# Kernel optimization log

Measured on AMD Instinct MI355X. Metric: run time of the kernel, lower is better.

The kernel has to match this reference:

```python
import jax, jax.numpy as jnp
import numpy as np

BN_EPS = 1e-5


def setup_inputs() -> dict:
    key = jax.random.key(0)
    ks = jax.random.split(key, 8)
    B, C, H, W = 8, 256, 64, 64
    Ci = 128
    x = jax.random.normal(ks[0], (B, C, H, W), dtype=jnp.float32)
    # 1x1 conv weights stored as [out, in] (kernel size 1 squeezed)
    sc = 1.0 / np.sqrt(C)
    g_w = jax.random.uniform(ks[1], (Ci, C), jnp.float32, -sc, sc)
    g_b = jax.random.uniform(ks[2], (Ci,), jnp.float32, -sc, sc)
    theta_w = jax.random.uniform(ks[3], (Ci, C), jnp.float32, -sc, sc)
    theta_b = jax.random.uniform(ks[4], (Ci,), jnp.float32, -sc, sc)
    phi_w = jax.random.uniform(ks[5], (Ci, C), jnp.float32, -sc, sc)
    phi_b = jax.random.uniform(ks[6], (Ci,), jnp.float32, -sc, sc)
    # W conv: normal(std=0.01) weight, zero bias (per _init_weights)
    W_w = 0.01 * jax.random.normal(ks[7], (C, Ci), dtype=jnp.float32)
    W_b = jnp.zeros((C,), dtype=jnp.float32)
    bn_gamma = jnp.ones((C,), dtype=jnp.float32)
    bn_beta = jnp.zeros((C,), dtype=jnp.float32)
    return {"x": x, "g_w": g_w, "g_b": g_b, "theta_w": theta_w, "theta_b": theta_b,
            "phi_w": phi_w, "phi_b": phi_b, "W_w": W_w, "W_b": W_b,
            "bn_gamma": bn_gamma, "bn_beta": bn_beta}


def reference(x, g_w, g_b, theta_w, theta_b, phi_w, phi_b, W_w, W_b, bn_gamma, bn_beta):
    B, C, H, W = x.shape
    xf = x.reshape(B, C, H * W)                                   # [B, C, N]
    # 1x1 convs == per-position channel GEMMs
    g_x = jnp.einsum('oc,bcn->bon', g_w, xf) + g_b[:, None]        # [B, Ci, N]
    th = jnp.einsum('oc,bcn->bon', theta_w, xf) + theta_b[:, None]
    ph = jnp.einsum('oc,bcn->bon', phi_w, xf) + phi_b[:, None]
    # theta^T phi : [B, N, N] dense attention scores
    f = jnp.einsum('bcn,bcm->bnm', th, ph)
    attn = jax.nn.softmax(f, axis=-1)
    # attention-weighted sum of g values -> [B, Ci, N]
    y = jnp.einsum('bnm,bcm->bcn', attn, g_x)
    # output 1x1 conv + BatchNorm2d (training-mode batch stats)
    wy = jnp.einsum('oc,bcn->bon', W_w, y) + W_b[:, None]          # [B, C, N]
    mean = jnp.mean(wy, axis=(0, 2), keepdims=True)
    var = jnp.var(wy, axis=(0, 2), keepdims=True)
    wy_bn = (wy - mean) * jax.lax.rsqrt(var + BN_EPS)
    wy_bn = wy_bn * bn_gamma[:, None] + bn_beta[:, None]
    z = wy_bn.reshape(B, C, H, W) + x
    return z
```

## Files before the change

### kernel.cpp

```cpp
#include <hip/hip_runtime.h>
#include <hip/hip_bf16.h>
#include <math.h>

#define B_   8
#define C_   256
#define CI_  128
#define N_   4096

typedef unsigned short ushort_t;
typedef unsigned int uint_t;
typedef __attribute__((ext_vector_type(8))) short short8;
typedef __attribute__((ext_vector_type(16))) float floatx16;

#define OFF_W3B  0ull
#define OFF_B3   196608ull
#define OFF_WCB  198144ull
#define OFF_XT   263680ull
#define OFF_THT  17040896ull
#define OFF_PHT  25429504ull
#define OFF_G16  33818112ull
#define OFF_LP   42206720ull
#define OFF_YPB  42468864ull
#define OFF_WY   263680ull
#define OFF_ST   59246080ull

__device__ __forceinline__ ushort_t f2bf(float x) {
  union { float f; uint_t u; } c; c.f = x;
  return (ushort_t)((c.u + 0x7fffu + ((c.u >> 16) & 1u)) >> 16);
}
__device__ __forceinline__ uint_t pkbf(float a, float b) {
  __hip_bfloat162 h = __float22bfloat162_rn(float2{a, b});
  union { __hip_bfloat162 h; uint_t u; } c; c.h = h; return c.u;
}
__device__ __forceinline__ float bf_lo(uint_t u) {
  union { uint_t u; float f; } c; c.u = u << 16; return c.f;
}
__device__ __forceinline__ float bf_hi(uint_t u) {
  union { uint_t u; float f; } c; c.u = u & 0xffff0000u; return c.f;
}
__device__ __forceinline__ void async_copy16(const void* g, void* l) {
  __builtin_amdgcn_global_load_lds(
      (const __attribute__((address_space(1))) unsigned int*)g,
      (__attribute__((address_space(3))) unsigned int*)l, 16, 0, 0);
}

__global__ __launch_bounds__(256) void pack_w(
    const float* __restrict__ g_w, const float* __restrict__ g_b,
    const float* __restrict__ th_w, const float* __restrict__ th_b,
    const float* __restrict__ ph_w, const float* __restrict__ ph_b,
    const float* __restrict__ W_w,
    ushort_t* __restrict__ W3b, float* __restrict__ b3,
    ushort_t* __restrict__ Wc)
{
  int bid = blockIdx.x;
  if (bid < 384) {
    int i = bid * 256 + threadIdx.x;
    int o = i >> 8;
    float v;
    if (o < 128)      v = g_w[i];
    else if (o < 256) v = th_w[i - 128*256];
    else              v = ph_w[i - 256*256];
    W3b[i] = f2bf(v);
    if ((i & 255) == 0)
      b3[o] = (o < 128) ? g_b[o] : (o < 256) ? th_b[o - 128] : ph_b[o - 256];
  } else {
    int j = (bid - 384) * 256 + threadIdx.x;
    Wc[j] = f2bf(W_w[j]);
  }
}

__global__ __launch_bounds__(256) void xcast(
    const float* __restrict__ x, ushort_t* __restrict__ xt)
{
  const int b = blockIdx.z, c0 = blockIdx.y * 64, n0 = blockIdx.x * 64;
  const int tid = threadIdx.x;
  __shared__ float xs[64][65];
  const int nq = (tid & 15) * 4, cr = tid >> 4;
  #pragma unroll
  for (int i = 0; i < 4; ++i) {
    float4 v = *(const float4*)&x[((size_t)b * C_ + c0 + cr + 16*i) * N_ + n0 + nq];
    xs[cr + 16*i][nq] = v.x; xs[cr + 16*i][nq+1] = v.y;
    xs[cr + 16*i][nq+2] = v.z; xs[cr + 16*i][nq+3] = v.w;
  }
  __syncthreads();
  const int n = tid >> 2, cs = (tid & 3) * 16;
  uint_t u[8];
  #pragma unroll
  for (int j = 0; j < 8; ++j)
    u[j] = pkbf(xs[cs + 2*j][n], xs[cs + 2*j + 1][n]);
  ushort_t* dst = &xt[((size_t)b * N_ + n0 + n) * C_ + c0 + cs];
  *(uint4*)dst       = make_uint4(u[0], u[1], u[2], u[3]);
  *(uint4*)(dst + 8) = make_uint4(u[4], u[5], u[6], u[7]);
}

__global__ __launch_bounds__(256, 2) void proj_all(
    const ushort_t* __restrict__ W3b, const float* __restrict__ b3,
    const ushort_t* __restrict__ xt, ushort_t* __restrict__ tht,
    ushort_t* __restrict__ pht, ushort_t* __restrict__ g16)
{
  const int b = blockIdx.z, nb = blockIdx.x, ot = blockIdx.y;
  const int gm = (ot == 2);
  const int o0 = gm ? 0 : (128 + ot * 128);
  const int tid = threadIdx.x, w = tid >> 6, lane = tid & 63;
  const int l31 = lane & 31, h = lane >> 5, xk = l31 & 7;
  __shared__ ushort_t ws_l[128 * 64];
  __shared__ ushort_t xs_l[128 * 64];
  const ushort_t* xb = xt + (size_t)b * N_ * C_;
  const int n0 = nb * 128;
  floatx16 acc[4];
  #pragma unroll
  for (int ct = 0; ct < 4; ++ct)
    #pragma unroll
    for (int r = 0; r < 16; ++r) acc[ct][r] = 0.f;

  const int gr = lane >> 3, gu = lane & 7;
  for (int k0 = 0; k0 < C_; k0 += 64) {
    __syncthreads();
    #pragma unroll
    for (int i = 0; i < 4; ++i) {
      int r = w*32 + i*8 + gr;
      async_copy16(&W3b[(size_t)(o0 + r) * C_ + k0 + ((gu ^ (r & 7)) * 8)],
                   &ws_l[(w*32 + i*8) * 64]);
      async_copy16(&xb[(size_t)(n0 + r) * C_ + k0 + ((gu ^ (r & 7)) * 8)],
                   &xs_l[(w*32 + i*8) * 64]);
    }
    __syncthreads();
    const ushort_t* bmat = gm ? ws_l : xs_l;
    const ushort_t* amat = gm ? xs_l : ws_l;
    #pragma unroll
    for (int kk = 0; kk < 4; ++kk) {
      int fc = ((2*kk + h) ^ xk) * 8;
      short8 bf = *(const short8*)&bmat[(w*32 + l31) * 64 + fc];
      #pragma unroll
      for (int ct = 0; ct < 4; ++ct) {
        short8 af = *(const short8*)&amat[(ct*32 + l31) * 64 + fc];
        acc[ct] = __builtin_amdgcn_mfma_f32_32x32x16_bf16(af, bf, acc[ct], 0, 0, 0);
      }
    }
  }

  if (gm) {
    float bv = b3[w*32 + l31];
    ushort_t* gp = g16 + ((size_t)b * CI_ + w*32 + l31) * N_;
    #pragma unroll
    for (int ct = 0; ct < 4; ++ct)
      #pragma unroll
      for (int rq = 0; rq < 4; ++rq) {
        uint2 d = make_uint2(pkbf(acc[ct][4*rq+0] + bv, acc[ct][4*rq+1] + bv),
                             pkbf(acc[ct][4*rq+2] + bv, acc[ct][4*rq+3] + bv));
        *(uint2*)&gp[n0 + ct*32 + 8*rq + 4*h] = d;
      }
  } else {
    ushort_t* tp = ((ot == 0) ? tht : pht) + ((size_t)b * N_ + n0 + w*32 + l31) * CI_;
    #pragma unroll
    for (int ct = 0; ct < 4; ++ct)
      #pragma unroll
      for (int rq = 0; rq < 4; ++rq) {
        float4 bv = *(const float4*)&b3[o0 + ct*32 + 8*rq + 4*h];
        uint2 d = make_uint2(pkbf(acc[ct][4*rq+0] + bv.x, acc[ct][4*rq+1] + bv.y),
                             pkbf(acc[ct][4*rq+2] + bv.z, acc[ct][4*rq+3] + bv.w));
        *(uint2*)&tp[ct*32 + 8*rq + 4*h] = d;
      }
  }
}

#define LOG2E_  1.442695041f
#define MBIAS_  (-28.85390082f)

__global__ __launch_bounds__(256, 2) void attn_mfma(
    const ushort_t* __restrict__ tht, const ushort_t* __restrict__ pht,
    const ushort_t* __restrict__ g16, ushort_t* __restrict__ yp,
    float* __restrict__ lp)
{
  const int b  = blockIdx.x & 7;
  const int ms = (blockIdx.x >> 3) & 1;
  const int qb = blockIdx.x >> 4;
  const int tid = threadIdx.x, w = tid >> 6, lane = tid & 63;
  const int l31 = lane & 31, h = lane >> 5, xk = l31 & 7;

  __shared__ ushort_t smem[40960];
  ushort_t* Plw = smem + 32768 + w * 2048;

  const int q0w = qb * 128 + w * 32;
  const int m_base = ms * 2048;

  const ushort_t* thb = tht + (size_t)b * N_ * CI_;
  const ushort_t* phb = pht + (size_t)b * N_ * CI_;
  const ushort_t* gbp = g16 + (size_t)b * CI_ * N_;

  short8 tf[8];
  #pragma unroll
  for (int kk = 0; kk < 8; ++kk)
    tf[kk] = *(const short8*)&thb[(size_t)(q0w + l31) * CI_ + kk*16 + h*8];

  floatx16 acc[4];
  #pragma unroll
  for (int ct = 0; ct < 4; ++ct)
    #pragma unroll
    for (int r = 0; r < 16; ++r) acc[ct][r] = 0.f;
  float lpart = 0.f;

  const int phr = lane >> 4, phu = lane & 15;
  const int gr  = lane >> 3, gu  = lane & 7;

  #define STAGE_ATTN(m0v, bufv)                                               \
    {                                                                         \
      ushort_t* phs_ = smem + (bufv) * 8192;                                  \
      ushort_t* gs_  = smem + 16384 + (bufv) * 8192;                          \
      _Pragma("unroll")                                                       \
      for (int i = 0; i < 4; ++i) {                                           \
        int row = w*16 + i*4 + phr;                                           \
        async_copy16(&phb[(size_t)((m0v) + row) * CI_ + ((phu ^ (row & 7)) * 8)], \
                     &phs_[(w*16 + i*4) * 128]);                              \
      }                                                                       \
      _Pragma("unroll")                                                       \
      for (int i = 0; i < 4; ++i) {                                           \
        int c = w*32 + i*8 + gr;                                              \
        async_copy16(&gbp[(size_t)c * N_ + (m0v) + ((gu ^ (c & 7)) * 8)],     \
                     &gs_[(w*32 + i*8) * 64]);                                \
      }                                                                       \
    }

  STAGE_ATTN(m_base, 0);
  asm volatile("s_waitcnt vmcnt(0)" ::: "memory");
  __builtin_amdgcn_s_barrier();

  #pragma unroll 2
  for (int it = 0; it < 32; ++it) {
    const int cur = it & 1;
    const int m0 = m_base + it * 64;
    if (it < 31) STAGE_ATTN(m0 + 64, cur ^ 1);
    const ushort_t* phs = smem + cur * 8192;
    const ushort_t* gs  = smem + 16384 + cur * 8192;

    #pragma unroll
    for (int mt = 0; mt < 2; ++mt) {
      floatx16 s;
      #pragma unroll
      for (int r = 0; r < 16; ++r) s[r] = 0.f;
      __builtin_amdgcn_s_setprio(1);
      #pragma unroll
      for (int kk = 0; kk < 8; ++kk) {
        short8 pf = *(const short8*)&phs[(mt*32 + l31) * 128 + (((2*kk + h) ^ xk) * 8)];
        s = __builtin_amdgcn_mfma_f32_32x32x16_bf16(pf, tf[kk], s, 0, 0, 0);
      }
      __builtin_amdgcn_s_setprio(0);
      float ls = 0.f;
      #pragma unroll
      for (int rq = 0; rq < 4; ++rq) {
        float p0 = exp2f(fmaf(s[4*rq+0], LOG2E_, MBIAS_));
        float p1 = exp2f(fmaf(s[4*rq+1], LOG2E_, MBIAS_));
        float p2 = exp2f(fmaf(s[4*rq+2], LOG2E_, MBIAS_));
        float p3 = exp2f(fmaf(s[4*rq+3], LOG2E_, MBIAS_));
        ls += (p0 + p1) + (p2 + p3);
        uint2 d = make_uint2(pkbf(p0, p1), pkbf(p2, p3));
        *(uint2*)&Plw[l31 * 64 + (((mt*4 + rq) ^ xk) * 8) + h*4] = d;
      }
      lpart += ls;
    }

    __builtin_amdgcn_s_setprio(1);
    #pragma unroll
    for (int kk = 0; kk < 4; ++kk) {
      int pc = ((2*kk + h) ^ xk) * 8;
      short8 pfr = *(const short8*)&Plw[l31 * 64 + pc];
      #pragma unroll
      for (int ct = 0; ct < 4; ++ct) {
        short8 gf = *(const short8*)&gs[(ct*32 + l31) * 64 + pc];
        acc[ct] = __builtin_amdgcn_mfma_f32_32x32x16_bf16(gf, pfr, acc[ct], 0, 0, 0);
      }
    }
    __builtin_amdgcn_s_setprio(0);

    asm volatile("s_waitcnt vmcnt(0)" ::: "memory");
    __builtin_amdgcn_s_barrier();
  }

  float lq = lpart + __shfl_xor(lpart, 32);
  if (h == 0)
    lp[((size_t)ms * 8 + b) * N_ + q0w + l31] = lq;

  __syncthreads();
  ushort_t* tr = smem + w * 4096;
  #pragma unroll
  for (int ct = 0; ct < 4; ++ct)
    #pragma unroll
    for (int rq = 0; rq < 4; ++rq) {
      uint2 d = make_uint2(pkbf(acc[ct][4*rq+0], acc[ct][4*rq+1]),
                           pkbf(acc[ct][4*rq+2], acc[ct][4*rq+3]));
      *(uint2*)&tr[l31 * 128 + ct*32 + 8*rq + 4*h] = d;
    }
  ushort_t* ypb = yp + (((size_t)ms * 8 + b) * N_ + q0w) * CI_;
  #pragma unroll
  for (int itx = 0; itx < 8; ++itx) {
    int row = itx*4 + (lane >> 4);
    int cu  = (lane & 15) * 8;
    uint4 v = *(const uint4*)&tr[row * 128 + cu];
    *(uint4*)&ypb[(size_t)row * CI_ + cu] = v;
  }
}

__global__ __launch_bounds__(256, 2) void wgemm_fused(
    const ushort_t* __restrict__ Wc, const float* __restrict__ Wb,
    const ushort_t* __restrict__ yp, const float* __restrict__ lp,
    float* __restrict__ WY)
{
  const int b = blockIdx.z, nb = blockIdx.x, ot = blockIdx.y;
  const int o0 = ot * 128;
  const int tid = threadIdx.x, w = tid >> 6, lane = tid & 63;
  const int l31 = lane & 31, h = lane >> 5, xk = l31 & 7;
  __shared__ ushort_t ws_l[128 * 64];
  __shared__ ushort_t xs_l[128 * 64];
  const int n0 = nb * 128;
  const size_t PH = (size_t)B_ * N_ * CI_;
  const ushort_t* yp0 = yp + (size_t)b * N_ * CI_;
  const ushort_t* yp1 = yp0 + PH;
  floatx16 acc[4];
  #pragma unroll
  for (int ct = 0; ct < 4; ++ct)
    #pragma unroll
    for (int r = 0; r < 16; ++r) acc[ct][r] = 0.f;

  const int gr = lane >> 3, gu = lane & 7;
  for (int k0 = 0; k0 < CI_; k0 += 64) {
    __syncthreads();
    #pragma unroll
    for (int i = 0; i < 4; ++i) {
      int r = w*32 + i*8 + gr;
      async_copy16(&Wc[(size_t)(o0 + r) * CI_ + k0 + ((gu ^ (r & 7)) * 8)],
                   &ws_l[(w*32 + i*8) * 64]);
      int n = n0 + r;
      size_t src = (size_t)n * CI_ + k0 + ((gu ^ (r & 7)) * 8);
      uint4 a0 = *(const uint4*)&yp0[src];
      uint4 a1 = *(const uint4*)&yp1[src];
      float inv = 1.0f / (lp[(size_t)b * N_ + n] + lp[(size_t)(8 + b) * N_ + n]);
      uint4 o;
      o.x = pkbf((bf_lo(a0.x) + bf_lo(a1.x)) * inv, (bf_hi(a0.x) + bf_hi(a1.x)) * inv);
      o.y = pkbf((bf_lo(a0.y) + bf_lo(a1.y)) * inv, (bf_hi(a0.y) + bf_hi(a1.y)) * inv);
      o.z = pkbf((bf_lo(a0.z) + bf_lo(a1.z)) * inv, (bf_hi(a0.z) + bf_hi(a1.z)) * inv);
      o.w = pkbf((bf_lo(a0.w) + bf_lo(a1.w)) * inv, (bf_hi(a0.w) + bf_hi(a1.w)) * inv);
      *(uint4*)&xs_l[r * 64 + gu * 8] = o;
    }
    __syncthreads();
    #pragma unroll
    for (int kk = 0; kk < 4; ++kk) {
      int fc = ((2*kk + h) ^ xk) * 8;
      short8 bf = *(const short8*)&xs_l[(w*32 + l31) * 64 + fc];
      #pragma unroll
      for (int ct = 0; ct < 4; ++ct) {
        short8 af = *(const short8*)&ws_l[(ct*32 + l31) * 64 + fc];
        acc[ct] = __builtin_amdgcn_mfma_f32_32x32x16_bf16(af, bf, acc[ct], 0, 0, 0);
      }
    }
  }
  const int n = n0 + w*32 + l31;
  #pragma unroll
  for (int ct = 0; ct < 4; ++ct)
    #pragma unroll
    for (int rq = 0; rq < 4; ++rq) {
      float4 bv = *(const float4*)&Wb[o0 + ct*32 + 8*rq + 4*h];
      #pragma unroll
      for (int j = 0; j < 4; ++j) {
        int o = o0 + ct*32 + 8*rq + 4*h + j;
        WY[((size_t)b * C_ + o) * N_ + n] = acc[ct][4*rq + j] + (&bv.x)[j];
      }
    }
}

__global__ __launch_bounds__(256) void bn_stats(
    const float* __restrict__ WY, float* __restrict__ st)
{
  const int o = blockIdx.x;
  const int tid = threadIdx.x;
  float s = 0.f, s2 = 0.f;
  for (int b = 0; b < B_; ++b) {
    const float* p = WY + ((size_t)b * C_ + o) * N_;
    for (int n = tid * 4; n < N_; n += 256 * 4) {
      float4 v = *(const float4*)&p[n];
      s  += v.x + v.y + v.z + v.w;
      s2 += v.x * v.x + v.y * v.y + v.z * v.z + v.w * v.w;
    }
  }
  __shared__ float rs[256], rs2[256];
  rs[tid] = s; rs2[tid] = s2;
  __syncthreads();
  for (int off = 128; off > 0; off >>= 1) {
    if (tid < off) { rs[tid] += rs[tid + off]; rs2[tid] += rs2[tid + off]; }
    __syncthreads();
  }
  if (tid == 0) {
    const float M = (float)(B_ * N_);
    float mean = rs[0] / M;
    float var  = rs2[0] / M - mean * mean;
    st[o] = mean;
    st[256 + o] = rsqrtf(var + 1e-5f);
  }
}

__global__ __launch_bounds__(256) void bn_apply(
    const float* __restrict__ WY, const float* __restrict__ x,
    const float* __restrict__ st, const float* __restrict__ gamma,
    const float* __restrict__ beta, float* __restrict__ out)
{
  size_t i = ((size_t)blockIdx.x * 256 + threadIdx.x) * 4;
  int o = (int)((i >> 12) & 255);
  float4 w  = *(const float4*)&WY[i];
  float4 xv = *(const float4*)&x[i];
  float gsc = gamma[o] * st[256 + o];
  float bb  = beta[o] - st[o] * gsc;
  float4 v;
  v.x = w.x * gsc + bb + xv.x;
  v.y = w.y * gsc + bb + xv.y;
  v.z = w.z * gsc + bb + xv.z;
  v.w = w.w * gsc + bb + xv.w;
  *(float4*)&out[i] = v;
}

extern "C" void kernel_launch(void* const* d_in, const int* in_sizes, int n_in,
                              void* d_out, int out_size, void* d_ws, size_t ws_size,
                              hipStream_t stream)
{
  const float* x       = (const float*)d_in[0];
  const float* g_w     = (const float*)d_in[1];
  const float* g_b     = (const float*)d_in[2];
  const float* theta_w = (const float*)d_in[3];
  const float* theta_b = (const float*)d_in[4];
  const float* phi_w   = (const float*)d_in[5];
  const float* phi_b   = (const float*)d_in[6];
  const float* W_w     = (const float*)d_in[7];
  const float* W_b     = (const float*)d_in[8];
  const float* gamma   = (const float*)d_in[9];
  const float* beta    = (const float*)d_in[10];
  float* out = (float*)d_out;

  char* ws = (char*)d_ws;
  ushort_t* W3b = (ushort_t*)(ws + OFF_W3B);
  float*    b3  = (float*)(ws + OFF_B3);
  ushort_t* Wc  = (ushort_t*)(ws + OFF_WCB);
  ushort_t* xt  = (ushort_t*)(ws + OFF_XT);
  ushort_t* tht = (ushort_t*)(ws + OFF_THT);
  ushort_t* pht = (ushort_t*)(ws + OFF_PHT);
  ushort_t* g16 = (ushort_t*)(ws + OFF_G16);
  float*    lpp = (float*)(ws + OFF_LP);
  ushort_t* ypb = (ushort_t*)(ws + OFF_YPB);
  float*    WY  = (float*)(ws + OFF_WY);
  float*    ST  = (float*)(ws + OFF_ST);

  pack_w<<<512, 256, 0, stream>>>(g_w, g_b, theta_w, theta_b, phi_w, phi_b,
                                  W_w, W3b, b3, Wc);
  xcast<<<dim3(64, 4, 8), 256, 0, stream>>>(x, xt);
  proj_all<<<dim3(32, 3, 8), 256, 0, stream>>>(W3b, b3, xt, tht, pht, g16);
  attn_mfma<<<512, 256, 0, stream>>>(tht, pht, g16, ypb, lpp);
  wgemm_fused<<<dim3(32, 2, 8), 256, 0, stream>>>(Wc, W_b, ypb, lpp, WY);
  bn_stats<<<256, 256, 0, stream>>>(WY, ST);
  bn_apply<<<8192, 256, 0, stream>>>(WY, x, ST, gamma, beta, out);
}
```

Baseline: 243.4 us.

## Keep softmax probabilities in registers via permlane32 swap instead of LDS round-trip

The exponentiated scores are packed to bf16 and rearranged across lane halves with permlane32_swap, so they feed the PV MFMA operand directly without being written to and re-read from shared memory. This removes the per-wave P staging buffer (8K ushorts of LDS) and its stores and loads. The two QK score tiles are also computed interleaved, giving two independent MFMA chains. The costs are extra cross-lane permute instructions and higher register pressure from holding two score accumulators at once.

```diff
diff --git a/kernel.cpp b/kernel.cpp
--- a/kernel.cpp
+++ b/kernel.cpp
@@ -11,6 +11,7 @@
 typedef unsigned int uint_t;
 typedef __attribute__((ext_vector_type(8))) short short8;
 typedef __attribute__((ext_vector_type(16))) float floatx16;
+typedef __attribute__((ext_vector_type(2))) unsigned int uint2v;
 
 #define OFF_W3B  0ull
 #define OFF_B3   196608ull
@@ -178,8 +179,7 @@
   const int tid = threadIdx.x, w = tid >> 6, lane = tid & 63;
   const int l31 = lane & 31, h = lane >> 5, xk = l31 & 7;
 
-  __shared__ ushort_t smem[40960];
-  ushort_t* Plw = smem + 32768 + w * 2048;
+  __shared__ ushort_t smem[32768];
 
   const int q0w = qb * 128 + w * 32;
   const int m_base = ms * 2048;
@@ -221,6 +221,38 @@
       }                                                                       \
     }
 
+  #define SMPV(sv, mtv)                                                       \
+    {                                                                         \
+      uint_t Aw[4], Bw[4];                                                    \
+      float ls = 0.f;                                                         \
+      _Pragma("unroll")                                                       \
+      for (int rq = 0; rq < 4; ++rq) {                                        \
+        float p0 = exp2f(fmaf(sv[4*rq+0], LOG2E_, MBIAS_));                   \
+        float p1 = exp2f(fmaf(sv[4*rq+1], LOG2E_, MBIAS_));                   \
+        float p2 = exp2f(fmaf(sv[4*rq+2], LOG2E_, MBIAS_));                   \
+        float p3 = exp2f(fmaf(sv[4*rq+3], LOG2E_, MBIAS_));                   \
+        ls += (p0 + p1) + (p2 + p3);                                          \
+        Aw[rq] = pkbf(p0, p1);                                                \
+        Bw[rq] = pkbf(p2, p3);                                                \
+      }                                                                       \
+      lpart += ls;                                                            \
+      _Pragma("unroll")                                                       \
+      for (int t = 0; t < 2; ++t) {                                           \
+        uint2v ra = __builtin_amdgcn_permlane32_swap(Aw[2*t], Aw[2*t+1], false, false); \
+        uint2v rb = __builtin_amdgcn_permlane32_swap(Bw[2*t], Bw[2*t+1], false, false); \
+        union { uint_t u[4]; short8 s; } pk_;                                 \
+        pk_.u[0] = ra.x; pk_.u[1] = rb.x; pk_.u[2] = ra.y; pk_.u[3] = rb.y;   \
+        const int pc = ((2*(2*(mtv) + t) + h) ^ xk) * 8;                      \
+        __builtin_amdgcn_s_setprio(1);                                        \
+        _Pragma("unroll")                                                     \
+        for (int ct = 0; ct < 4; ++ct) {                                      \
+          short8 gf = *(const short8*)&gs[(ct*32 + l31) * 64 + pc];           \
+          acc[ct] = __builtin_amdgcn_mfma_f32_32x32x16_bf16(gf, pk_.s, acc[ct], 0, 0, 0); \
+        }                                                                     \
+        __builtin_amdgcn_s_setprio(0);                                        \
+      }                                                                       \
+    }
+
   STAGE_ATTN(m_base, 0);
   asm volatile("s_waitcnt vmcnt(0)" ::: "memory");
   __builtin_amdgcn_s_barrier();
@@ -233,44 +265,22 @@
     const ushort_t* phs = smem + cur * 8192;
     const ushort_t* gs  = smem + 16384 + cur * 8192;
 
-    #pragma unroll
-    for (int mt = 0; mt < 2; ++mt) {
-      floatx16 s;
-      #pragma unroll
-      for (int r = 0; r < 16; ++r) s[r] = 0.f;
-      __builtin_amdgcn_s_setprio(1);
-      #pragma unroll
-      for (int kk = 0; kk < 8; ++kk) {
-        short8 pf = *(const short8*)&phs[(mt*32 + l31) * 128 + (((2*kk + h) ^ xk) * 8)];
-        s = __builtin_amdgcn_mfma_f32_32x32x16_bf16(pf, tf[kk], s, 0, 0, 0);
-      }
-      __builtin_amdgcn_s_setprio(0);
-      float ls = 0.f;
-      #pragma unroll
-      for (int rq = 0; rq < 4; ++rq) {
-        float p0 = exp2f(fmaf(s[4*rq+0], LOG2E_, MBIAS_));
-        float p1 = exp2f(fmaf(s[4*rq+1], LOG2E_, MBIAS_));
-        float p2 = exp2f(fmaf(s[4*rq+2], LOG2E_, MBIAS_));
-        float p3 = exp2f(fmaf(s[4*rq+3], LOG2E_, MBIAS_));
-        ls += (p0 + p1) + (p2 + p3);
-        uint2 d = make_uint2(pkbf(p0, p1), pkbf(p2, p3));
-        *(uint2*)&Plw[l31 * 64 + (((mt*4 + rq) ^ xk) * 8) + h*4] = d;
-      }
-      lpart += ls;
-    }
-
+    floatx16 s0, s1;
+    #pragma unroll
+    for (int r = 0; r < 16; ++r) { s0[r] = 0.f; s1[r] = 0.f; }
     __builtin_amdgcn_s_setprio(1);
     #pragma unroll
-    for (int kk = 0; kk < 4; ++kk) {
-      int pc = ((2*kk + h) ^ xk) * 8;
-      short8 pfr = *(const short8*)&Plw[l31 * 64 + pc];
-      #pragma unroll
-      for (int ct = 0; ct < 4; ++ct) {
-        short8 gf = *(const short8*)&gs[(ct*32 + l31) * 64 + pc];
-        acc[ct] = __builtin_amdgcn_mfma_f32_32x32x16_bf16(gf, pfr, acc[ct], 0, 0, 0);
-      }
+    for (int kk = 0; kk < 8; ++kk) {
+      const int fc = (((2*kk + h) ^ xk) * 8);
+      short8 pf0 = *(const short8*)&phs[(l31) * 128 + fc];
+      s0 = __builtin_amdgcn_mfma_f32_32x32x16_bf16(pf0, tf[kk], s0, 0, 0, 0);
+      short8 pf1 = *(const short8*)&phs[(32 + l31) * 128 + fc];
+      s1 = __builtin_amdgcn_mfma_f32_32x32x16_bf16(pf1, tf[kk], s1, 0, 0, 0);
     }
     __builtin_amdgcn_s_setprio(0);
+
+    SMPV(s0, 0)
+    SMPV(s1, 1)
 
     asm volatile("s_waitcnt vmcnt(0)" ::: "memory");
     __builtin_amdgcn_s_barrier();
```

New measurement: 253.0 us. 4.0% more time.

## Split attention keys four ways, keep P in registers via permlane swap, bf16 WY

Applied to the files above, without the earlier changes.

The attention kernel now splits the key range into four chunks instead of two and uses 32-key tiles, which roughly halves shared memory and raises occupancy to 4 blocks per SU. The softmax probabilities are rearranged with permlane32_swap and fed straight into the PV MFMA, so the LDS round-trip for P goes away. A raw v_exp_f32 replaces exp2f. Row sums are combined with atomicAdd into a buffer that pack_w now zeroes. The output of the W projection is stored as bf16, which halves the traffic for the BN stats and apply passes. In exchange, the four partial y buffers add more reads in wgemm, and storing WY in bf16 lowers precision.

```diff
diff --git a/kernel.cpp b/kernel.cpp
--- a/kernel.cpp
+++ b/kernel.cpp
@@ -11,18 +11,20 @@
 typedef unsigned int uint_t;
 typedef __attribute__((ext_vector_type(8))) short short8;
 typedef __attribute__((ext_vector_type(16))) float floatx16;
-
-#define OFF_W3B  0ull
-#define OFF_B3   196608ull
-#define OFF_WCB  198144ull
-#define OFF_XT   263680ull
-#define OFF_THT  17040896ull
-#define OFF_PHT  25429504ull
-#define OFF_G16  33818112ull
-#define OFF_LP   42206720ull
-#define OFF_YPB  42468864ull
-#define OFF_WY   263680ull
-#define OFF_ST   59246080ull
+typedef __attribute__((ext_vector_type(2))) unsigned int uint2v;
+
+#define OFF_W3B   0ull
+#define OFF_B3    196608ull
+#define OFF_WCB   198144ull
+#define OFF_LP    263680ull
+#define OFF_ST    394752ull
+#define OFF_THT   396800ull
+#define OFF_PHT   8785408ull
+#define OFF_G16   17174016ull
+#define OFF_XT    25562624ull
+#define OFF_YP23  25562624ull
+#define OFF_YP01  42339840ull
+#define OFF_WY    396800ull
 
 __device__ __forceinline__ ushort_t f2bf(float x) {
   union { float f; uint_t u; } c; c.f = x;
@@ -37,6 +39,9 @@
 }
 __device__ __forceinline__ float bf_hi(uint_t u) {
   union { uint_t u; float f; } c; c.u = u & 0xffff0000u; return c.f;
+}
+__device__ __forceinline__ float fexp2(float x) {
+  float r; asm("v_exp_f32 %0, %1\ns_nop 0" : "=v"(r) : "v"(x)); return r;
 }
 __device__ __forceinline__ void async_copy16(const void* g, void* l) {
   __builtin_amdgcn_global_load_lds(
@@ -50,7 +55,7 @@
     const float* __restrict__ ph_w, const float* __restrict__ ph_b,
     const float* __restrict__ W_w,
     ushort_t* __restrict__ W3b, float* __restrict__ b3,
-    ushort_t* __restrict__ Wc)
+    ushort_t* __restrict__ Wc, float* __restrict__ lp)
 {
   int bid = blockIdx.x;
   if (bid < 384) {
@@ -63,9 +68,11 @@
     W3b[i] = f2bf(v);
     if ((i & 255) == 0)
       b3[o] = (o < 128) ? g_b[o] : (o < 256) ? th_b[o - 128] : ph_b[o - 256];
-  } else {
+  } else if (bid < 512) {
     int j = (bid - 384) * 256 + threadIdx.x;
     Wc[j] = f2bf(W_w[j]);
+  } else {
+    lp[(bid - 512) * 256 + threadIdx.x] = 0.f;
   }
 }
 
@@ -167,22 +174,22 @@
 #define LOG2E_  1.442695041f
 #define MBIAS_  (-28.85390082f)
 
-__global__ __launch_bounds__(256, 2) void attn_mfma(
+__global__ __launch_bounds__(256, 4) void attn_mfma(
     const ushort_t* __restrict__ tht, const ushort_t* __restrict__ pht,
-    const ushort_t* __restrict__ g16, ushort_t* __restrict__ yp,
-    float* __restrict__ lp)
+    const ushort_t* __restrict__ g16, ushort_t* __restrict__ ypA,
+    ushort_t* __restrict__ ypB, float* __restrict__ lp)
 {
   const int b  = blockIdx.x & 7;
-  const int ms = (blockIdx.x >> 3) & 1;
-  const int qb = blockIdx.x >> 4;
+  const int ms = (blockIdx.x >> 3) & 3;
+  const int qb = blockIdx.x >> 5;
   const int tid = threadIdx.x, w = tid >> 6, lane = tid & 63;
   const int l31 = lane & 31, h = lane >> 5, xk = l31 & 7;
-
-  __shared__ ushort_t smem[40960];
-  ushort_t* Plw = smem + 32768 + w * 2048;
+  const int xk2 = (l31 >> 1) & 3;
+
+  __shared__ ushort_t smem[16384];
 
   const int q0w = qb * 128 + w * 32;
-  const int m_base = ms * 2048;
+  const int m_base = ms * 1024;
 
   const ushort_t* thb = tht + (size_t)b * N_ * CI_;
   const ushort_t* phb = pht + (size_t)b * N_ * CI_;
@@ -201,23 +208,23 @@
   float lpart = 0.f;
 
   const int phr = lane >> 4, phu = lane & 15;
-  const int gr  = lane >> 3, gu  = lane & 7;
+  const int g_r = lane >> 2, g_u = lane & 3;
 
   #define STAGE_ATTN(m0v, bufv)                                               \
     {                                                                         \
-      ushort_t* phs_ = smem + (bufv) * 8192;                                  \
-      ushort_t* gs_  = smem + 16384 + (bufv) * 8192;                          \
+      ushort_t* phs_ = smem + (bufv) * 4096;                                  \
+      ushort_t* gs_  = smem + 8192 + (bufv) * 4096;                           \
       _Pragma("unroll")                                                       \
-      for (int i = 0; i < 4; ++i) {                                           \
-        int row = w*16 + i*4 + phr;                                           \
+      for (int i = 0; i < 2; ++i) {                                           \
+        int row = w*8 + i*4 + phr;                                            \
         async_copy16(&phb[(size_t)((m0v) + row) * CI_ + ((phu ^ (row & 7)) * 8)], \
-                     &phs_[(w*16 + i*4) * 128]);                              \
+                     &phs_[(w*8 + i*4) * 128]);                               \
       }                                                                       \
       _Pragma("unroll")                                                       \
-      for (int i = 0; i < 4; ++i) {                                           \
-        int c = w*32 + i*8 + gr;                                              \
-        async_copy16(&gbp[(size_t)c * N_ + (m0v) + ((gu ^ (c & 7)) * 8)],     \
-                     &gs_[(w*32 + i*8) * 64]);                                \
+      for (int i = 0; i < 2; ++i) {                                           \
+        int c = (w*2 + i) * 16 + g_r;                                         \
+        async_copy16(&gbp[(size_t)c * N_ + (m0v) + ((g_u ^ ((c >> 1) & 3)) * 8)], \
+                     &gs_[(w*2 + i) * 512]);                                  \
       }                                                                       \
     }
 
@@ -228,49 +235,51 @@
   #pragma unroll 2
   for (int it = 0; it < 32; ++it) {
     const int cur = it & 1;
-    const int m0 = m_base + it * 64;
-    if (it < 31) STAGE_ATTN(m0 + 64, cur ^ 1);
-    const ushort_t* phs = smem + cur * 8192;
-    const ushort_t* gs  = smem + 16384 + cur * 8192;
-
-    #pragma unroll
-    for (int mt = 0; mt < 2; ++mt) {
-      floatx16 s;
-      #pragma unroll
-      for (int r = 0; r < 16; ++r) s[r] = 0.f;
+    const int m0 = m_base + it * 32;
+    if (it < 31) STAGE_ATTN(m0 + 32, cur ^ 1);
+    const ushort_t* phs = smem + cur * 4096;
+    const ushort_t* gs  = smem + 8192 + cur * 4096;
+
+    floatx16 s;
+    #pragma unroll
+    for (int r = 0; r < 16; ++r) s[r] = 0.f;
+    __builtin_amdgcn_s_setprio(1);
+    #pragma unroll
+    for (int kk = 0; kk < 8; ++kk) {
+      short8 pf = *(const short8*)&phs[l31 * 128 + (((2*kk + h) ^ xk) * 8)];
+      s = __builtin_amdgcn_mfma_f32_32x32x16_bf16(pf, tf[kk], s, 0, 0, 0);
+    }
+    __builtin_amdgcn_s_setprio(0);
+
+    uint_t Aw[4], Bw[4];
+    float ls = 0.f;
+    #pragma unroll
+    for (int rq = 0; rq < 4; ++rq) {
+      float p0 = fexp2(fmaf(s[4*rq+0], LOG2E_, MBIAS_));
+      float p1 = fexp2(fmaf(s[4*rq+1], LOG2E_, MBIAS_));
+      float p2 = fexp2(fmaf(s[4*rq+2], LOG2E_, MBIAS_));
+      float p3 = fexp2(fmaf(s[4*rq+3], LOG2E_, MBIAS_));
+      ls += (p0 + p1) + (p2 + p3);
+      Aw[rq] = pkbf(p0, p1);
+      Bw[rq] = pkbf(p2, p3);
+    }
+    lpart += ls;
+
+    #pragma unroll
+    for (int t = 0; t < 2; ++t) {
+      uint2v ra = __builtin_amdgcn_permlane32_swap(Aw[2*t], Aw[2*t+1], false, false);
+      uint2v rb = __builtin_amdgcn_permlane32_swap(Bw[2*t], Bw[2*t+1], false, false);
+      union { uint_t u[4]; short8 s; } pk_;
+      pk_.u[0] = ra.x; pk_.u[1] = rb.x; pk_.u[2] = ra.y; pk_.u[3] = rb.y;
+      const int pc = (((2*t + h) ^ xk2) * 8);
       __builtin_amdgcn_s_setprio(1);
       #pragma unroll
-      for (int kk = 0; kk < 8; ++kk) {
-        short8 pf = *(const short8*)&phs[(mt*32 + l31) * 128 + (((2*kk + h) ^ xk) * 8)];
-        s = __builtin_amdgcn_mfma_f32_32x32x16_bf16(pf, tf[kk], s, 0, 0, 0);
+      for (int ct = 0; ct < 4; ++ct) {
+        short8 gf = *(const short8*)&gs[(ct*32 + l31) * 32 + pc];
+        acc[ct] = __builtin_amdgcn_mfma_f32_32x32x16_bf16(gf, pk_.s, acc[ct], 0, 0, 0);
       }
       __builtin_amdgcn_s_setprio(0);
-      float ls = 0.f;
-      #pragma unroll
-      for (int rq = 0; rq < 4; ++rq) {
-        float p0 = exp2f(fmaf(s[4*rq+0], LOG2E_, MBIAS_));
-        float p1 = exp2f(fmaf(s[4*rq+1], LOG2E_, MBIAS_));
-        float p2 = exp2f(fmaf(s[4*rq+2], LOG2E_, MBIAS_));
-        float p3 = exp2f(fmaf(s[4*rq+3], LOG2E_, MBIAS_));
-        ls += (p0 + p1) + (p2 + p3);
-        uint2 d = make_uint2(pkbf(p0, p1), pkbf(p2, p3));
-        *(uint2*)&Plw[l31 * 64 + (((mt*4 + rq) ^ xk) * 8) + h*4] = d;
-      }
-      lpart += ls;
-    }
-
-    __builtin_amdgcn_s_setprio(1);
-    #pragma unroll
-    for (int kk = 0; kk < 4; ++kk) {
-      int pc = ((2*kk + h) ^ xk) * 8;
-      short8 pfr = *(const short8*)&Plw[l31 * 64 + pc];
-      #pragma unroll
-      for (int ct = 0; ct < 4; ++ct) {
-        short8 gf = *(const short8*)&gs[(ct*32 + l31) * 64 + pc];
-        acc[ct] = __builtin_amdgcn_mfma_f32_32x32x16_bf16(gf, pfr, acc[ct], 0, 0, 0);
-      }
-    }
-    __builtin_amdgcn_s_setprio(0);
+    }
 
     asm volatile("s_waitcnt vmcnt(0)" ::: "memory");
     __builtin_amdgcn_s_barrier();
@@ -278,7 +287,7 @@
 
   float lq = lpart + __shfl_xor(lpart, 32);
   if (h == 0)
-    lp[((size_t)ms * 8 + b) * N_ + q0w + l31] = lq;
+    atomicAdd(&lp[(size_t)b * N_ + q0w + l31], lq);
 
   __syncthreads();
   ushort_t* tr = smem + w * 4096;
@@ -290,7 +299,8 @@
                            pkbf(acc[ct][4*rq+2], acc[ct][4*rq+3]));
       *(uint2*)&tr[l31 * 128 + ct*32 + 8*rq + 4*h] = d;
     }
-  ushort_t* ypb = yp + (((size_t)ms * 8 + b) * N_ + q0w) * CI_;
+  ushort_t* ypb = ((ms < 2) ? ypA : ypB)
+                + (((size_t)(ms & 1) * B_ + b) * N_ + q0w) * CI_;
   #pragma unroll
   for (int itx = 0; itx < 8; ++itx) {
     int row = itx*4 + (lane >> 4);
@@ -302,8 +312,8 @@
 
 __global__ __launch_bounds__(256, 2) void wgemm_fused(
     const ushort_t* __restrict__ Wc, const float* __restrict__ Wb,
-    const ushort_t* __restrict__ yp, const float* __restrict__ lp,
-    float* __restrict__ WY)
+    const ushort_t* __restrict__ ypA, const ushort_t* __restrict__ ypB,
+    const float* __restrict__ lp, ushort_t* __restrict__ WYb)
 {
   const int b = blockIdx.z, nb = blockIdx.x, ot = blockIdx.y;
   const int o0 = ot * 128;
@@ -313,8 +323,10 @@
   __shared__ ushort_t xs_l[128 * 64];
   const int n0 = nb * 128;
   const size_t PH = (size_t)B_ * N_ * CI_;
-  const ushort_t* yp0 = yp + (size_t)b * N_ * CI_;
+  const ushort_t* yp0 = ypA + (size_t)b * N_ * CI_;
   const ushort_t* yp1 = yp0 + PH;
+  const ushort_t* yp2 = ypB + (size_t)b * N_ * CI_;
+  const ushort_t* yp3 = yp2 + PH;
   floatx16 acc[4];
   #pragma unroll
   for (int ct = 0; ct < 4; ++ct)
@@ -333,12 +345,18 @@
       size_t src = (size_t)n * CI_ + k0 + ((gu ^ (r & 7)) * 8);
       uint4 a0 = *(const uint4*)&yp0[src];
       uint4 a1 = *(const uint4*)&yp1[src];
-      float inv = 1.0f / (lp[(size_t)b * N_ + n] + lp[(size_t)(8 + b) * N_ + n]);
+      uint4 a2 = *(const uint4*)&yp2[src];
+      uint4 a3 = *(const uint4*)&yp3[src];
+      float inv = 1.0f / lp[(size_t)b * N_ + n];
       uint4 o;
-      o.x = pkbf((bf_lo(a0.x) + bf_lo(a1.x)) * inv, (bf_hi(a0.x) + bf_hi(a1.x)) * inv);
-      o.y = pkbf((bf_lo(a0.y) + bf_lo(a1.y)) * inv, (bf_hi(a0.y) + bf_hi(a1.y)) * inv);
-      o.z = pkbf((bf_lo(a0.z) + bf_lo(a1.z)) * inv, (bf_hi(a0.z) + bf_hi(a1.z)) * inv);
-      o.w = pkbf((bf_lo(a0.w) + bf_lo(a1.w)) * inv, (bf_hi(a0.w) + bf_hi(a1.w)) * inv);
+      o.x = pkbf((bf_lo(a0.x)+bf_lo(a1.x)+bf_lo(a2.x)+bf_lo(a3.x)) * inv,
+                 (bf_hi(a0.x)+bf_hi(a1.x)+bf_hi(a2.x)+bf_hi(a3.x)) * inv);
+      o.y = pkbf((bf_lo(a0.y)+bf_lo(a1.y)+bf_lo(a2.y)+bf_lo(a3.y)) * inv,
+                 (bf_hi(a0.y)+bf_hi(a1.y)+bf_hi(a2.y)+bf_hi(a3.y)) * inv);
+      o.z = pkbf((bf_lo(a0.z)+bf_lo(a1.z)+bf_lo(a2.z)+bf_lo(a3.z)) * inv,
+                 (bf_hi(a0.z)+bf_hi(a1.z)+bf_hi(a2.z)+bf_hi(a3.z)) * inv);
+      o.w = pkbf((bf_lo(a0.w)+bf_lo(a1.w)+bf_lo(a2.w)+bf_lo(a3.w)) * inv,
+                 (bf_hi(a0.w)+bf_hi(a1.w)+bf_hi(a2.w)+bf_hi(a3.w)) * inv);
       *(uint4*)&xs_l[r * 64 + gu * 8] = o;
     }
     __syncthreads();
@@ -362,23 +380,25 @@
       #pragma unroll
       for (int j = 0; j < 4; ++j) {
         int o = o0 + ct*32 + 8*rq + 4*h + j;
-        WY[((size_t)b * C_ + o) * N_ + n] = acc[ct][4*rq + j] + (&bv.x)[j];
+        WYb[((size_t)b * C_ + o) * N_ + n] = f2bf(acc[ct][4*rq + j] + (&bv.x)[j]);
       }
     }
 }
 
 __global__ __launch_bounds__(256) void bn_stats(
-    const float* __restrict__ WY, float* __restrict__ st)
+    const ushort_t* __restrict__ WYb, float* __restrict__ st)
 {
   const int o = blockIdx.x;
   const int tid = threadIdx.x;
   float s = 0.f, s2 = 0.f;
   for (int b = 0; b < B_; ++b) {
-    const float* p = WY + ((size_t)b * C_ + o) * N_;
-    for (int n = tid * 4; n < N_; n += 256 * 4) {
-      float4 v = *(const float4*)&p[n];
-      s  += v.x + v.y + v.z + v.w;
-      s2 += v.x * v.x + v.y * v.y + v.z * v.z + v.w * v.w;
+    const ushort_t* p = WYb + ((size_t)b * C_ + o) * N_;
+    for (int n = tid * 8; n < N_; n += 256 * 8) {
+      uint4 v = *(const uint4*)&p[n];
+      float f0 = bf_lo(v.x), f1 = bf_hi(v.x), f2 = bf_lo(v.y), f3 = bf_hi(v.y);
+      float f4 = bf_lo(v.z), f5 = bf_hi(v.z), f6 = bf_lo(v.w), f7 = bf_hi(v.w);
+      s  += ((f0 + f1) + (f2 + f3)) + ((f4 + f5) + (f6 + f7));
+      s2 += ((f0*f0 + f1*f1) + (f2*f2 + f3*f3)) + ((f4*f4 + f5*f5) + (f6*f6 + f7*f7));
     }
   }
   __shared__ float rs[256], rs2[256];
@@ -398,21 +418,21 @@
 }
 
 __global__ __launch_bounds__(256) void bn_apply(
-    const float* __restrict__ WY, const float* __restrict__ x,
+    const ushort_t* __restrict__ WYb, const float* __restrict__ x,
     const float* __restrict__ st, const float* __restrict__ gamma,
     const float* __restrict__ beta, float* __restrict__ out)
 {
   size_t i = ((size_t)blockIdx.x * 256 + threadIdx.x) * 4;
   int o = (int)((i >> 12) & 255);
-  float4 w  = *(const float4*)&WY[i];
+  uint2 wv = *(const uint2*)&WYb[i];
   float4 xv = *(const float4*)&x[i];
   float gsc = gamma[o] * st[256 + o];
   float bb  = beta[o] - st[o] * gsc;
   float4 v;
-  v.x = w.x * gsc + bb + xv.x;
-  v.y = w.y * gsc + bb + xv.y;
-  v.z = w.z * gsc + bb + xv.z;
-  v.w = w.w * gsc + bb + xv.w;
+  v.x = bf_lo(wv.x) * gsc + bb + xv.x;
+  v.y = bf_hi(wv.x) * gsc + bb + xv.y;
+  v.z = bf_lo(wv.y) * gsc + bb + xv.z;
+  v.w = bf_hi(wv.y) * gsc + bb + xv.w;
   *(float4*)&out[i] = v;
 }
 
@@ -437,21 +457,22 @@
   ushort_t* W3b = (ushort_t*)(ws + OFF_W3B);
   float*    b3  = (float*)(ws + OFF_B3);
   ushort_t* Wc  = (ushort_t*)(ws + OFF_WCB);
-  ushort_t* xt  = (ushort_t*)(ws + OFF_XT);
+  float*    lpp = (float*)(ws + OFF_LP);
+  float*    ST  = (float*)(ws + OFF_ST);
   ushort_t* tht = (ushort_t*)(ws + OFF_THT);
   ushort_t* pht = (ushort_t*)(ws + OFF_PHT);
   ushort_t* g16 = (ushort_t*)(ws + OFF_G16);
-  float*    lpp = (float*)(ws + OFF_LP);
-  ushort_t* ypb = (ushort_t*)(ws + OFF_YPB);
-  float*    WY  = (float*)(ws + OFF_WY);
-  float*    ST  = (float*)(ws + OFF_ST);
-
-  pack_w<<<512, 256, 0, stream>>>(g_w, g_b, theta_w, theta_b, phi_w, phi_b,
-                                  W_w, W3b, b3, Wc);
+  ushort_t* xt  = (ushort_t*)(ws + OFF_XT);
+  ushort_t* ypA = (ushort_t*)(ws + OFF_YP01);
+  ushort_t* ypB = (ushort_t*)(ws + OFF_YP23);
+  ushort_t* WYb = (ushort_t*)(ws + OFF_WY);
+
+  pack_w<<<640, 256, 0, stream>>>(g_w, g_b, theta_w, theta_b, phi_w, phi_b,
+                                  W_w, W3b, b3, Wc, lpp);
   xcast<<<dim3(64, 4, 8), 256, 0, stream>>>(x, xt);
   proj_all<<<dim3(32, 3, 8), 256, 0, stream>>>(W3b, b3, xt, tht, pht, g16);
-  attn_mfma<<<512, 256, 0, stream>>>(tht, pht, g16, ypb, lpp);
-  wgemm_fused<<<dim3(32, 2, 8), 256, 0, stream>>>(Wc, W_b, ypb, lpp, WY);
-  bn_stats<<<256, 256, 0, stream>>>(WY, ST);
-  bn_apply<<<8192, 256, 0, stream>>>(WY, x, ST, gamma, beta, out);
-}
+  attn_mfma<<<1024, 256, 0, stream>>>(tht, pht, g16, ypA, ypB, lpp);
+  wgemm_fused<<<dim3(32, 2, 8), 256, 0, stream>>>(Wc, W_b, ypA, ypB, lpp, WYb);
+  bn_stats<<<256, 256, 0, stream>>>(WYb, ST);
+  bn_apply<<<8192, 256, 0, stream>>>(WYb, x, ST, gamma, beta, out);
+}
```

After: 301.6 us. +23.9%, slower.
